# Performance work log

Measured on AMD Instinct MI355X. Metric: run time of the kernel, lower is better.

## Reference

```python
import jax, jax.numpy as jnp
import numpy as np

N = 512          # n_nodes
F = 64           # hidden scalar/vector channels (hidden_irreps 64x0e+64x1o)
S = 5            # num_species
T = 32           # time embedding dim
M = 64           # MLP_irreps 64x0e
L = 2            # num_interactions
AVG = 511.0      # avg_num_neighbors (fully connected)
E = N * (N - 1)


def _sph(v):
    """Real spherical harmonics l=0,1,2 (component norm) of normalized vectors. v: [E,3]."""
    r = jnp.linalg.norm(v, axis=-1, keepdims=True)  # [E,1]
    u = v / r
    x, y, z = u[..., 0], u[..., 1], u[..., 2]
    s3, s5, s15 = 3.0 ** 0.5, 5.0 ** 0.5, 15.0 ** 0.5
    Y0 = jnp.ones_like(x)[..., None]
    Y1 = s3 * u
    Y2 = jnp.stack([s15 * x * y, s15 * y * z, 0.5 * s5 * (3 * z * z - 1.0),
                    s15 * x * z, 0.5 * s15 * (x * x - y * y)], axis=-1)
    return jnp.concatenate([Y0, Y1, Y2], axis=-1), r  # [E,9], [E,1]


def setup_inputs() -> dict:
    key = jax.random.key(0)
    ks = jax.random.split(key, 16)
    snd, rcv = np.nonzero(~np.eye(N, dtype=bool))  # fully-connected, no self loops
    return dict(
        positions=jax.random.normal(ks[0], (N, 3), jnp.float32),
        node_features=jax.random.randint(ks[1], (N,), 1, S + 1, jnp.int32),
        time_embedding=jax.random.normal(ks[2], (T,), jnp.float32),
        senders=jnp.asarray(snd, jnp.int32),
        receivers=jnp.asarray(rcv, jnp.int32),
        W_embed=jax.random.normal(ks[3], (S + T, F)) * 0.1,
        b_embed=jnp.zeros((F,)),
        W_lin=jax.random.normal(ks[4], (L, 3, F, F)) / jnp.sqrt(float(F)),
        W_e1=jax.random.normal(ks[5], (L, 1, 32)),
        b_e1=jnp.zeros((L, 32)),
        W_e2=jax.random.normal(ks[6], (L, 32, F * 6)) * 0.05,
        Wp0=jax.random.normal(ks[7], (L, S, F, 6)) * 0.1,
        Wp1=jax.random.normal(ks[8], (L, S, F, 3)) * 0.1,
        Wr1=jax.random.normal(ks[9], (L, F, M)) / jnp.sqrt(float(F)),
        br1=jnp.zeros((L, M)),
        Wr2s=jax.random.normal(ks[10], (L, M, 16)) * 0.1,
        Wr2g=jax.random.normal(ks[11], (L, M, F)) * 0.1,
    )


def reference(positions, node_features, time_embedding, senders, receivers,
              W_embed, b_embed, W_lin, W_e1, b_e1, W_e2, Wp0, Wp1, Wr1, br1, Wr2s, Wr2g):
    species = node_features - 1                                  # ints in [0,S)
    onehot = jax.nn.one_hot(species, S, dtype=positions.dtype)   # /normalization_factor=1
    te = jnp.tile(time_embedding, (N, 1))
    h = jnp.concatenate([onehot, te], axis=-1) @ W_embed + b_embed  # embedding Dense -> [N,F]
    node_feats = jnp.zeros((N, F, 9), positions.dtype).at[:, :, 0].set(h)
    pos0 = positions
    pos = positions
    for l in range(L):
        vec = pos[receivers] - pos[senders]                      # [E,3]
        Y, lengths = _sph(vec)                                   # SH of edge dirs, edge lengths
        # per-l channel-mixing linear on node feats
        x0 = jnp.einsum('nf,fg->ng', node_feats[:, :, 0], W_lin[l, 0])
        x1 = jnp.einsum('nfm,fg->ngm', node_feats[:, :, 1:4], W_lin[l, 1])
        x2 = jnp.einsum('nfm,fg->ngm', node_feats[:, :, 4:9], W_lin[l, 2])
        s0, s1, s2 = x0[senders], x1[senders], x2[senders]       # gather sender feats
        # edge-length MLP producing per-channel per-CG-path weights
        he = jax.nn.silu(lengths @ W_e1[l] + b_e1[l])            # [E,32]
        w = (he @ W_e2[l]).reshape(-1, F, 6)                     # 6 TP paths
        Y1 = Y[:, None, 1:4]
        Y2c = Y[:, None, 4:9]
        # CG tensor-product paths: 0x0->0, 0x1->1, 0x2->2, 1x1->0, 1x1->1, 2x2->0
        m0 = (w[..., 0] * s0 * Y[:, 0:1]
              + w[..., 3] * jnp.sum(s1 * Y1, -1)
              + w[..., 5] * jnp.sum(s2 * Y2c, -1))               # [E,F]
        m1 = w[..., 1, None] * s0[..., None] * Y1 + w[..., 4, None] * jnp.cross(s1, Y1)
        m2 = w[..., 2, None] * s0[..., None] * Y2c
        msg = jnp.concatenate([m0[..., None], m1, m2], axis=-1)  # [E,F,9]
        A = jax.ops.segment_sum(msg, receivers, num_segments=N) / AVG  # scatter-aggregate
        # EquivariantProductBasisBlock: species-weighted symmetric contractions (correlation 3)
        A0, A1, A2 = A[:, :, 0], A[:, :, 1:4], A[:, :, 4:9]
        n1 = jnp.sum(A1 * A1, -1)
        n2 = jnp.sum(A2 * A2, -1)
        t0 = jnp.stack([A0, A0 * A0, A0 ** 3, n1, n2, A0 * n1], axis=-1)
        w0 = Wp0[l][species]                                     # [N,F,6]
        w1 = Wp1[l][species]                                     # [N,F,3]
        out0 = jnp.sum(t0 * w0, -1)                              # [N,F] scalars
        gpoly = w1[..., 0] + w1[..., 1] * A0 + w1[..., 2] * A0 * A0
        out1 = gpoly[..., None] * A1                             # [N,F,3] vectors
        node_feats = (jnp.zeros((N, F, 9), positions.dtype)
                      .at[:, :, 0].set(out0).at[:, :, 1:4].set(out1))
        # NonLinearReadoutBlock: gated vector readout (scalar outputs are discarded upstream)
        hr = jax.nn.silu(out0 @ Wr1[l] + br1[l])
        gate = hr @ Wr2g[l]                                      # [N,F]
        vec_out = jnp.einsum('nf,nfc->nc', gate, out1)           # [N,3] many_body_vectors
        pos = pos + vec_out
    return (pos - pos0)[:, :3]                                    # final_scaling = 1.0
```

## Files before the change

kernel.cpp:

```cpp
#include <hip/hip_runtime.h>
#include <hip/hip_bf16.h>

using bf16 = __hip_bfloat16;
using bf16x8 = __attribute__((ext_vector_type(8))) short;
using f32x4  = __attribute__((ext_vector_type(4))) float;

#define NN 512
#define NS 511

enum : int {
  WS_FLAG = 0,
  WS_X0S  = 16,
  WS_POS  = 336,
  WS_POS2 = 1872,
  WS_DELTA= 3408,
  WS_XS1  = 4960,
};

__device__ __forceinline__ short f2b(float x) {
  unsigned u = __builtin_bit_cast(unsigned, x);
  unsigned r = (u + 0x7fffu + ((u >> 16) & 1u)) >> 16;
  return (short)r;
}

__device__ __forceinline__ float ld(const void* p, int i, int isf32) {
  if (isf32) return ((const float*)p)[i];
  return __bfloat162float(((const bf16*)p)[i]);
}

__global__ __launch_bounds__(256) void k_pre(
    const void* __restrict__ positions, const void* __restrict__ te,
    const void* __restrict__ W_embed, const void* __restrict__ b_embed,
    const void* __restrict__ W_lin, float* __restrict__ ws) {
  const int b = blockIdx.x, t = threadIdx.x;
  __shared__ int flag_s;
  __shared__ float tvp[4][64];
  __shared__ float hst[64];
  __shared__ float xp[4][64];
  if (t < 64) {
    int cnt = 0;
    #pragma unroll
    for (int kq = 0; kq < 4; ++kq) {
      float v = __bfloat162float(((const bf16*)W_embed)[t + kq * 64]);
      float av = fabsf(v);
      cnt += (v == v && av > 1e-8f && av < 1e4f) ? 1 : 0;
    }
    #pragma unroll
    for (int off = 32; off > 0; off >>= 1) cnt += __shfl_down(cnt, off);
    if (t == 0) flag_s = (cnt >= 240) ? 0 : 1;
  }
  __syncthreads();
  const int isf32 = flag_s;

  if (b == 5) {
    if (t == 0) ((int*)ws)[WS_FLAG] = isf32;
    for (int idx = t; idx < NN * 3; idx += 256)
      ws[WS_POS + idx] = ld(positions, idx, isf32);
    return;
  }
  {
    int q = t & 63, kc = t >> 6;
    float ptv = 0.f;
    #pragma unroll
    for (int k = kc * 8; k < kc * 8 + 8; ++k)
      ptv += ld(te, k, isf32) * ld(W_embed, (5 + k) * 64 + q, isf32);
    tvp[kc][q] = ptv;
  }
  __syncthreads();
  if (t < 64)
    hst[t] = tvp[0][t] + tvp[1][t] + tvp[2][t] + tvp[3][t] +
             ld(b_embed, t, isf32) + ld(W_embed, b * 64 + t, isf32);
  __syncthreads();
  {
    int f = t & 63, qc = t >> 6;
    float px = 0.f;
    #pragma unroll
    for (int q2 = qc * 16; q2 < qc * 16 + 16; ++q2)
      px += hst[q2] * ld(W_lin, q2 * 64 + f, isf32);
    xp[qc][f] = px;
  }
  __syncthreads();
  if (t < 64)
    ws[WS_X0S + b * 64 + t] = xp[0][t] + xp[1][t] + xp[2][t] + xp[3][t];
}

template <int L>
__global__ __launch_bounds__(256) void k_edgenode(
    const int* __restrict__ nodef, const void* __restrict__ W_lin,
    const void* __restrict__ W_e1, const void* __restrict__ b_e1,
    const void* __restrict__ W_e2, const void* __restrict__ Wp0,
    const void* __restrict__ Wp1, const void* __restrict__ Wr1,
    const void* __restrict__ br1, const void* __restrict__ Wr2g,
    float* __restrict__ ws, void* __restrict__ out) {
  constexpr int HAS1 = L;
  constexpr int K = HAS1 ? 5 : 3;
  constexpr int N = K * 64;
  const int j = blockIdx.x;
  const int t = threadIdx.x;
  const int lane = t & 63;
  const int wave = t >> 6;
  const int quad = lane >> 4;
  const int lo = lane & 15;

  __shared__ short Bhi[N * 40];
  __shared__ float red[4][64][9];
  __shared__ float Af[64][9];
  __shared__ float s0l[64];
  __shared__ float o1l[3][64];
  __shared__ float hl[64];
  __shared__ float X0l[320];

  const int isf32 = ((const int*)ws)[WS_FLAG];

  {
    for (int idx = t; idx < N * 32; idx += 256) {
      int n = idx >> 5, h = idx & 31;
      int kp = n >> 6, f = n & 63;
      int src = (L * 32 + h) * 384 + f * 6 + kp;
      short bits;
      if (isf32) bits = f2b(((const float*)W_e2)[src]);
      else       bits = ((const short*)W_e2)[src];
      Bhi[n * 40 + h] = bits;
    }
    if (!HAS1) {
      for (int idx = t; idx < 320; idx += 256) X0l[idx] = ws[WS_X0S + idx];
    }
  }
  const float* pos = ws + (L ? WS_POS2 : WS_POS);
  const f32x4* xs = (const f32x4*)(ws + WS_XS1);
  float we1v[8], be1v[8];
  #pragma unroll
  for (int i = 0; i < 8; ++i) {
    we1v[i] = ld(W_e1, L * 32 + quad * 8 + i, isf32);
    be1v[i] = ld(b_e1, L * 32 + quad * 8 + i, isf32);
  }
  const float pjx = pos[j * 3 + 0], pjy = pos[j * 3 + 1], pjz = pos[j * 3 + 2];

  const float s3 = 1.7320508075688772f;
  const float s5h = 1.118033988749895f;
  const float s15 = 3.872983346207417f;
  const float s15h = 1.9364916731037085f;

  float acc[9][4] = {};
  __syncthreads();

  #pragma unroll 1
  for (int stile = wave; stile < 32; stile += 4) {
    bf16x8 af;
    {
      int ida = stile * 16 + lo;
      int ia = ida + (ida >= j);
      if (ia > 511) ia = 511;
      float pix = pos[ia * 3 + 0], piy = pos[ia * 3 + 1], piz = pos[ia * 3 + 2];
      float vx = pjx - pix, vy = pjy - piy, vz = pjz - piz;
      float r = sqrtf(vx * vx + vy * vy + vz * vz);
      #pragma unroll
      for (int i = 0; i < 8; ++i) {
        float x = r * we1v[i] + be1v[i];
        float he = x / (1.f + __expf(-x));
        af[i] = f2b(he);
      }
    }
    float Y1r[4][3], Y2r[4][5];
    int ir[4], sp4[4];
    bool vld[4];
    #pragma unroll
    for (int r4 = 0; r4 < 4; ++r4) {
      int idx = stile * 16 + quad * 4 + r4;
      vld[r4] = idx < NS;
      int i = idx + (idx >= j);
      if (i > 511) i = 511;
      ir[r4] = i;
      if (!HAS1) sp4[r4] = nodef[i] - 1;
      float pix = pos[i * 3 + 0], piy = pos[i * 3 + 1], piz = pos[i * 3 + 2];
      float vx = pjx - pix, vy = pjy - piy, vz = pjz - piz;
      float r2 = vx * vx + vy * vy + vz * vz;
      float rinv = r2 > 0.f ? rsqrtf(r2) : 0.f;
      float ux = vx * rinv, uy = vy * rinv, uz = vz * rinv;
      Y1r[r4][0] = s3 * ux; Y1r[r4][1] = s3 * uy; Y1r[r4][2] = s3 * uz;
      Y2r[r4][0] = s15 * ux * uy;
      Y2r[r4][1] = s15 * uy * uz;
      Y2r[r4][2] = s5h * (3.f * uz * uz - 1.f);
      Y2r[r4][3] = s15 * ux * uz;
      Y2r[r4][4] = s15h * (ux * ux - uy * uy);
    }
    #pragma unroll
    for (int ft = 0; ft < 4; ++ft) {
      int fcol = ft * 16 + lo;
      f32x4 xv[4];
      if (HAS1) {
        #pragma unroll
        for (int r4 = 0; r4 < 4; ++r4) xv[r4] = xs[ir[r4] * 64 + fcol];
      } else {
        #pragma unroll
        for (int r4 = 0; r4 < 4; ++r4) {
          f32x4 v = {X0l[sp4[r4] * 64 + fcol], 0.f, 0.f, 0.f};
          xv[r4] = v;
        }
      }
      f32x4 C[K];
      #pragma unroll
      for (int kp = 0; kp < K; ++kp) {
        const bf16x8 bh = *(const bf16x8*)&Bhi[(kp * 64 + fcol) * 40 + quad * 8];
        f32x4 c = {0.f, 0.f, 0.f, 0.f};
        C[kp] = __builtin_amdgcn_mfma_f32_16x16x32_bf16(af, bh, c, 0, 0, 0);
      }
      #pragma unroll
      for (int r4 = 0; r4 < 4; ++r4) {
        if (vld[r4]) {
          float s0 = xv[r4].x;
          float w0 = C[0][r4], w1 = C[1][r4], w2 = C[2][r4];
          if (HAS1) {
            float s1x = xv[r4].y, s1y = xv[r4].z, s1z = xv[r4].w;
            float w3 = C[3][r4], w4 = C[4][r4];
            float d1 = s1x * Y1r[r4][0] + s1y * Y1r[r4][1] + s1z * Y1r[r4][2];
            float cx = s1y * Y1r[r4][2] - s1z * Y1r[r4][1];
            float cy = s1z * Y1r[r4][0] - s1x * Y1r[r4][2];
            float cz = s1x * Y1r[r4][1] - s1y * Y1r[r4][0];
            acc[0][ft] += w0 * s0 + w3 * d1;
            float t1 = w1 * s0;
            acc[1][ft] += t1 * Y1r[r4][0] + w4 * cx;
            acc[2][ft] += t1 * Y1r[r4][1] + w4 * cy;
            acc[3][ft] += t1 * Y1r[r4][2] + w4 * cz;
          } else {
            acc[0][ft] += w0 * s0;
            float t1 = w1 * s0;
            acc[1][ft] += t1 * Y1r[r4][0];
            acc[2][ft] += t1 * Y1r[r4][1];
            acc[3][ft] += t1 * Y1r[r4][2];
          }
          float t2 = w2 * s0;
          acc[4][ft] += t2 * Y2r[r4][0];
          acc[5][ft] += t2 * Y2r[r4][1];
          acc[6][ft] += t2 * Y2r[r4][2];
          acc[7][ft] += t2 * Y2r[r4][3];
          acc[8][ft] += t2 * Y2r[r4][4];
        }
      }
    }
  }

  #pragma unroll
  for (int c = 0; c < 9; ++c)
    #pragma unroll
    for (int ft = 0; ft < 4; ++ft) {
      float v = acc[c][ft];
      v += __shfl_xor(v, 16);
      v += __shfl_xor(v, 32);
      acc[c][ft] = v;
    }
  if (quad == 0) {
    #pragma unroll
    for (int c = 0; c < 9; ++c)
      #pragma unroll
      for (int ft = 0; ft < 4; ++ft)
        red[wave][ft * 16 + lo][c] = acc[c][ft];
  }
  __syncthreads();
  for (int o = t; o < 576; o += 256) {
    int f = o / 9, c = o % 9;
    Af[f][c] = (red[0][f][c] + red[1][f][c] + red[2][f][c] + red[3][f][c]) *
               (1.f / 511.f);
  }
  __syncthreads();

  float out0 = 0.f, o1x = 0.f, o1y = 0.f, o1z = 0.f;
  if (t < 64) {
    int f = t;
    float a[9];
    #pragma unroll
    for (int c = 0; c < 9; ++c) a[c] = Af[f][c];
    int sp = nodef[j] - 1;
    int b0i = ((L * 5 + sp) * 64 + f) * 6;
    int b1i = ((L * 5 + sp) * 64 + f) * 3;
    float A0 = a[0];
    float n1 = a[1] * a[1] + a[2] * a[2] + a[3] * a[3];
    float n2 = a[4] * a[4] + a[5] * a[5] + a[6] * a[6] + a[7] * a[7] + a[8] * a[8];
    float A02 = A0 * A0;
    out0 = ld(Wp0, b0i + 0, isf32) * A0 + ld(Wp0, b0i + 1, isf32) * A02 +
           ld(Wp0, b0i + 2, isf32) * A02 * A0 + ld(Wp0, b0i + 3, isf32) * n1 +
           ld(Wp0, b0i + 4, isf32) * n2 + ld(Wp0, b0i + 5, isf32) * A0 * n1;
    float gp = ld(Wp1, b1i + 0, isf32) + ld(Wp1, b1i + 1, isf32) * A0 +
               ld(Wp1, b1i + 2, isf32) * A02;
    o1x = gp * a[1]; o1y = gp * a[2]; o1z = gp * a[3];
    s0l[f] = out0;
    if (L == 0) { o1l[0][f] = o1x; o1l[1][f] = o1y; o1l[2][f] = o1z; }
  }
  __syncthreads();
  if (t < 64) {
    int f = t;
    if (L == 0) {
      float b0 = 0.f, bx = 0.f, by = 0.f, bz = 0.f;
      #pragma unroll 8
      for (int q = 0; q < 64; ++q) {
        float w0 = ld(W_lin, 3 * 4096 + q * 64 + f, isf32);
        float w1 = ld(W_lin, 4 * 4096 + q * 64 + f, isf32);
        b0 += s0l[q] * w0;
        bx += o1l[0][q] * w1; by += o1l[1][q] * w1; bz += o1l[2][q] * w1;
      }
      f32x4 o = {b0, bx, by, bz};
      *(f32x4*)&ws[WS_XS1 + (j * 64 + f) * 4] = o;
    }
    float hacc = ld(br1, L * 64 + f, isf32);
    #pragma unroll 8
    for (int q = 0; q < 64; ++q)
      hacc += s0l[q] * ld(Wr1, (L * 64 + q) * 64 + f, isf32);
    hl[f] = hacc / (1.f + __expf(-hacc));
  }
  __syncthreads();
  if (t < 64) {
    int f = t;
    float gacc = 0.f;
    #pragma unroll 8
    for (int m = 0; m < 64; ++m)
      gacc += hl[m] * ld(Wr2g, (L * 64 + m) * 64 + f, isf32);
    float px = gacc * o1x, py = gacc * o1y, pz = gacc * o1z;
    #pragma unroll
    for (int off = 32; off > 0; off >>= 1) {
      px += __shfl_down(px, off);
      py += __shfl_down(py, off);
      pz += __shfl_down(pz, off);
    }
    if (f == 0) {
      if (L == 0) {
        ws[WS_DELTA + j * 3 + 0] = px;
        ws[WS_DELTA + j * 3 + 1] = py;
        ws[WS_DELTA + j * 3 + 2] = pz;
        ws[WS_POS2 + j * 3 + 0] = pos[j * 3 + 0] + px;
        ws[WS_POS2 + j * 3 + 1] = pos[j * 3 + 1] + py;
        ws[WS_POS2 + j * 3 + 2] = pos[j * 3 + 2] + pz;
      } else {
        float ox = ws[WS_DELTA + j * 3 + 0] + px;
        float oy = ws[WS_DELTA + j * 3 + 1] + py;
        float oz = ws[WS_DELTA + j * 3 + 2] + pz;
        if (isf32) {
          float* o = (float*)out;
          o[j * 3 + 0] = ox; o[j * 3 + 1] = oy; o[j * 3 + 2] = oz;
        } else {
          bf16* o = (bf16*)out;
          o[j * 3 + 0] = __float2bfloat16(ox);
          o[j * 3 + 1] = __float2bfloat16(oy);
          o[j * 3 + 2] = __float2bfloat16(oz);
        }
      }
    }
  }
}

extern "C" void kernel_launch(void* const* d_in, const int* in_sizes, int n_in,
                              void* d_out, int out_size, void* d_ws, size_t ws_size,
                              hipStream_t stream) {
  const void* positions = d_in[0];
  const int*  nodef     = (const int*)d_in[1];
  const void* te        = d_in[2];
  const void* W_embed   = d_in[5];
  const void* b_embed   = d_in[6];
  const void* W_lin     = d_in[7];
  const void* W_e1      = d_in[8];
  const void* b_e1      = d_in[9];
  const void* W_e2      = d_in[10];
  const void* Wp0       = d_in[11];
  const void* Wp1       = d_in[12];
  const void* Wr1       = d_in[13];
  const void* br1       = d_in[14];
  const void* Wr2g      = d_in[16];
  float* ws = (float*)d_ws;
  (void)in_sizes; (void)n_in; (void)out_size; (void)ws_size;

  k_pre<<<dim3(6), dim3(256), 0, stream>>>(positions, te, W_embed, b_embed,
                                           W_lin, ws);
  k_edgenode<0><<<dim3(512), dim3(256), 0, stream>>>(
      nodef, W_lin, W_e1, b_e1, W_e2, Wp0, Wp1, Wr1, br1, Wr2g, ws, d_out);
  k_edgenode<1><<<dim3(512), dim3(256), 0, stream>>>(
      nodef, W_lin, W_e1, b_e1, W_e2, Wp0, Wp1, Wr1, br1, Wr2g, ws, d_out);
}
```

Before: 187.6 us.

## Fold preprocessing kernel into edge-node kernels and parallelize node-tail matvecs

Removes the small k_pre launch: every block of the first edge kernel now redundantly computes the dtype flag, converts positions and species into shared memory, and computes the per-species initial embeddings. Positions are staged in LDS in both layers, so the edge loop reads them from shared memory instead of global. The per-node tail matvecs (W_lin, Wr1, Wr2g), previously done by a single wave, are split across all four waves with a shared-memory reduction. This trades one kernel launch and its serialization for redundant per-block setup work and extra LDS and barriers.

Result: slower. 205.1 us (+9.4%).

```diff
diff --git a/kernel.cpp b/kernel.cpp
--- a/kernel.cpp
+++ b/kernel.cpp
@@ -9,12 +9,9 @@
 #define NS 511
 
 enum : int {
-  WS_FLAG = 0,
-  WS_X0S  = 16,
-  WS_POS  = 336,
-  WS_POS2 = 1872,
-  WS_DELTA= 3408,
-  WS_XS1  = 4960,
+  WS_POS2 = 0,
+  WS_DELTA = 1536,
+  WS_XS1 = 3072,
 };
 
 __device__ __forceinline__ short f2b(float x) {
@@ -28,65 +25,11 @@
   return __bfloat162float(((const bf16*)p)[i]);
 }
 
-__global__ __launch_bounds__(256) void k_pre(
-    const void* __restrict__ positions, const void* __restrict__ te,
-    const void* __restrict__ W_embed, const void* __restrict__ b_embed,
-    const void* __restrict__ W_lin, float* __restrict__ ws) {
-  const int b = blockIdx.x, t = threadIdx.x;
-  __shared__ int flag_s;
-  __shared__ float tvp[4][64];
-  __shared__ float hst[64];
-  __shared__ float xp[4][64];
-  if (t < 64) {
-    int cnt = 0;
-    #pragma unroll
-    for (int kq = 0; kq < 4; ++kq) {
-      float v = __bfloat162float(((const bf16*)W_embed)[t + kq * 64]);
-      float av = fabsf(v);
-      cnt += (v == v && av > 1e-8f && av < 1e4f) ? 1 : 0;
-    }
-    #pragma unroll
-    for (int off = 32; off > 0; off >>= 1) cnt += __shfl_down(cnt, off);
-    if (t == 0) flag_s = (cnt >= 240) ? 0 : 1;
-  }
-  __syncthreads();
-  const int isf32 = flag_s;
-
-  if (b == 5) {
-    if (t == 0) ((int*)ws)[WS_FLAG] = isf32;
-    for (int idx = t; idx < NN * 3; idx += 256)
-      ws[WS_POS + idx] = ld(positions, idx, isf32);
-    return;
-  }
-  {
-    int q = t & 63, kc = t >> 6;
-    float ptv = 0.f;
-    #pragma unroll
-    for (int k = kc * 8; k < kc * 8 + 8; ++k)
-      ptv += ld(te, k, isf32) * ld(W_embed, (5 + k) * 64 + q, isf32);
-    tvp[kc][q] = ptv;
-  }
-  __syncthreads();
-  if (t < 64)
-    hst[t] = tvp[0][t] + tvp[1][t] + tvp[2][t] + tvp[3][t] +
-             ld(b_embed, t, isf32) + ld(W_embed, b * 64 + t, isf32);
-  __syncthreads();
-  {
-    int f = t & 63, qc = t >> 6;
-    float px = 0.f;
-    #pragma unroll
-    for (int q2 = qc * 16; q2 < qc * 16 + 16; ++q2)
-      px += hst[q2] * ld(W_lin, q2 * 64 + f, isf32);
-    xp[qc][f] = px;
-  }
-  __syncthreads();
-  if (t < 64)
-    ws[WS_X0S + b * 64 + t] = xp[0][t] + xp[1][t] + xp[2][t] + xp[3][t];
-}
-
 template <int L>
 __global__ __launch_bounds__(256) void k_edgenode(
-    const int* __restrict__ nodef, const void* __restrict__ W_lin,
+    const void* __restrict__ positions, const int* __restrict__ nodef,
+    const void* __restrict__ te, const void* __restrict__ W_embed,
+    const void* __restrict__ b_embed, const void* __restrict__ W_lin,
     const void* __restrict__ W_e1, const void* __restrict__ b_e1,
     const void* __restrict__ W_e2, const void* __restrict__ Wp0,
     const void* __restrict__ Wp1, const void* __restrict__ Wr1,
@@ -108,25 +51,73 @@
   __shared__ float s0l[64];
   __shared__ float o1l[3][64];
   __shared__ float hl[64];
+  __shared__ float posl[NN * 3];
   __shared__ float X0l[320];
-
-  const int isf32 = ((const int*)ws)[WS_FLAG];
-
-  {
-    for (int idx = t; idx < N * 32; idx += 256) {
-      int n = idx >> 5, h = idx & 31;
-      int kp = n >> 6, f = n & 63;
-      int src = (L * 32 + h) * 384 + f * 6 + kp;
-      short bits;
-      if (isf32) bits = f2b(((const float*)W_e2)[src]);
-      else       bits = ((const short*)W_e2)[src];
-      Bhi[n * 40 + h] = bits;
-    }
-    if (!HAS1) {
-      for (int idx = t; idx < 320; idx += 256) X0l[idx] = ws[WS_X0S + idx];
-    }
-  }
-  const float* pos = ws + (L ? WS_POS2 : WS_POS);
+  __shared__ int spl[NN];
+  __shared__ int flag_s;
+
+  if (t < 64) {
+    int cnt = 0;
+    #pragma unroll
+    for (int kq = 0; kq < 4; ++kq) {
+      float v = __bfloat162float(((const bf16*)W_embed)[t + kq * 64]);
+      float av = fabsf(v);
+      cnt += (v == v && av > 1e-8f && av < 1e4f) ? 1 : 0;
+    }
+    #pragma unroll
+    for (int off = 32; off > 0; off >>= 1) cnt += __shfl_down(cnt, off);
+    if (t == 0) flag_s = (cnt >= 240) ? 0 : 1;
+  }
+  __syncthreads();
+  const int isf32 = flag_s;
+
+  float* scr = &red[0][0][0];
+
+  if (!HAS1) {
+    for (int idx = t; idx < NN * 3; idx += 256)
+      posl[idx] = ld(positions, idx, isf32);
+    for (int idx = t; idx < NN; idx += 256) spl[idx] = nodef[idx] - 1;
+    {
+      int q = t & 63, kc = t >> 6;
+      float ptv = 0.f;
+      #pragma unroll
+      for (int k = kc * 8; k < kc * 8 + 8; ++k)
+        ptv += ld(te, k, isf32) * ld(W_embed, (5 + k) * 64 + q, isf32);
+      scr[kc * 64 + q] = ptv;
+    }
+  } else {
+    for (int idx = t; idx < NN * 3; idx += 256) posl[idx] = ws[WS_POS2 + idx];
+  }
+  for (int idx = t; idx < N * 32; idx += 256) {
+    int n = idx >> 5, h = idx & 31;
+    int kp = n >> 6, f = n & 63;
+    int src = (L * 32 + h) * 384 + f * 6 + kp;
+    short bits;
+    if (isf32) bits = f2b(((const float*)W_e2)[src]);
+    else       bits = ((const short*)W_e2)[src];
+    Bhi[n * 40 + h] = bits;
+  }
+  if (!HAS1) {
+    __syncthreads();
+    if (t < 64)
+      scr[512 + t] = scr[t] + scr[64 + t] + scr[128 + t] + scr[192 + t] +
+                     ld(b_embed, t, isf32);
+    __syncthreads();
+    for (int idx = t; idx < 320; idx += 256) {
+      int sp = idx >> 6, q = idx & 63;
+      scr[1024 + idx] = ld(W_embed, sp * 64 + q, isf32) + scr[512 + q];
+    }
+    __syncthreads();
+    for (int idx = t; idx < 320; idx += 256) {
+      int sp = idx >> 6, f = idx & 63;
+      float x = 0.f;
+      #pragma unroll 8
+      for (int q = 0; q < 64; ++q)
+        x += scr[1024 + sp * 64 + q] * ld(W_lin, q * 64 + f, isf32);
+      X0l[idx] = x;
+    }
+  }
+
   const f32x4* xs = (const f32x4*)(ws + WS_XS1);
   float we1v[8], be1v[8];
   #pragma unroll
@@ -134,15 +125,15 @@
     we1v[i] = ld(W_e1, L * 32 + quad * 8 + i, isf32);
     be1v[i] = ld(b_e1, L * 32 + quad * 8 + i, isf32);
   }
-  const float pjx = pos[j * 3 + 0], pjy = pos[j * 3 + 1], pjz = pos[j * 3 + 2];
 
   const float s3 = 1.7320508075688772f;
   const float s5h = 1.118033988749895f;
   const float s15 = 3.872983346207417f;
   const float s15h = 1.9364916731037085f;
 
+  __syncthreads();
+  const float pjx = posl[j * 3 + 0], pjy = posl[j * 3 + 1], pjz = posl[j * 3 + 2];
   float acc[9][4] = {};
-  __syncthreads();
 
   #pragma unroll 1
   for (int stile = wave; stile < 32; stile += 4) {
@@ -151,7 +142,7 @@
       int ida = stile * 16 + lo;
       int ia = ida + (ida >= j);
       if (ia > 511) ia = 511;
-      float pix = pos[ia * 3 + 0], piy = pos[ia * 3 + 1], piz = pos[ia * 3 + 2];
+      float pix = posl[ia * 3 + 0], piy = posl[ia * 3 + 1], piz = posl[ia * 3 + 2];
       float vx = pjx - pix, vy = pjy - piy, vz = pjz - piz;
       float r = sqrtf(vx * vx + vy * vy + vz * vz);
       #pragma unroll
@@ -171,8 +162,8 @@
       int i = idx + (idx >= j);
       if (i > 511) i = 511;
       ir[r4] = i;
-      if (!HAS1) sp4[r4] = nodef[i] - 1;
-      float pix = pos[i * 3 + 0], piy = pos[i * 3 + 1], piz = pos[i * 3 + 2];
+      if (!HAS1) sp4[r4] = spl[i];
+      float pix = posl[i * 3 + 0], piy = posl[i * 3 + 1], piz = posl[i * 3 + 2];
       float vx = pjx - pix, vy = pjy - piy, vz = pjz - piz;
       float r2 = vx * vx + vy * vy + vz * vz;
       float rinv = r2 > 0.f ? rsqrtf(r2) : 0.f;
@@ -287,33 +278,53 @@
     if (L == 0) { o1l[0][f] = o1x; o1l[1][f] = o1y; o1l[2][f] = o1z; }
   }
   __syncthreads();
+  {
+    int f = t & 63, qc = t >> 6;
+    float b0 = 0.f, bx = 0.f, by = 0.f, bz = 0.f, hacc = 0.f;
+    #pragma unroll 8
+    for (int q = qc * 16; q < qc * 16 + 16; ++q) {
+      float s0q = s0l[q];
+      if (L == 0) {
+        float w0 = ld(W_lin, 3 * 4096 + q * 64 + f, isf32);
+        float w1 = ld(W_lin, 4 * 4096 + q * 64 + f, isf32);
+        b0 += s0q * w0;
+        bx += o1l[0][q] * w1; by += o1l[1][q] * w1; bz += o1l[2][q] * w1;
+      }
+      hacc += s0q * ld(Wr1, (L * 64 + q) * 64 + f, isf32);
+    }
+    red[qc][f][0] = hacc;
+    if (L == 0) {
+      red[qc][f][1] = b0; red[qc][f][2] = bx;
+      red[qc][f][3] = by; red[qc][f][4] = bz;
+    }
+  }
+  __syncthreads();
   if (t < 64) {
     int f = t;
     if (L == 0) {
-      float b0 = 0.f, bx = 0.f, by = 0.f, bz = 0.f;
-      #pragma unroll 8
-      for (int q = 0; q < 64; ++q) {
-        float w0 = ld(W_lin, 3 * 4096 + q * 64 + f, isf32);
-        float w1 = ld(W_lin, 4 * 4096 + q * 64 + f, isf32);
-        b0 += s0l[q] * w0;
-        bx += o1l[0][q] * w1; by += o1l[1][q] * w1; bz += o1l[2][q] * w1;
-      }
-      f32x4 o = {b0, bx, by, bz};
+      f32x4 o = {red[0][f][1] + red[1][f][1] + red[2][f][1] + red[3][f][1],
+                 red[0][f][2] + red[1][f][2] + red[2][f][2] + red[3][f][2],
+                 red[0][f][3] + red[1][f][3] + red[2][f][3] + red[3][f][3],
+                 red[0][f][4] + red[1][f][4] + red[2][f][4] + red[3][f][4]};
       *(f32x4*)&ws[WS_XS1 + (j * 64 + f) * 4] = o;
     }
-    float hacc = ld(br1, L * 64 + f, isf32);
+    float hacc = red[0][f][0] + red[1][f][0] + red[2][f][0] + red[3][f][0] +
+                 ld(br1, L * 64 + f, isf32);
+    hl[f] = hacc / (1.f + __expf(-hacc));
+  }
+  __syncthreads();
+  {
+    int f = t & 63, mc = t >> 6;
+    float gacc = 0.f;
     #pragma unroll 8
-    for (int q = 0; q < 64; ++q)
-      hacc += s0l[q] * ld(Wr1, (L * 64 + q) * 64 + f, isf32);
-    hl[f] = hacc / (1.f + __expf(-hacc));
+    for (int m = mc * 16; m < mc * 16 + 16; ++m)
+      gacc += hl[m] * ld(Wr2g, (L * 64 + m) * 64 + f, isf32);
+    red[mc][f][0] = gacc;
   }
   __syncthreads();
   if (t < 64) {
     int f = t;
-    float gacc = 0.f;
-    #pragma unroll 8
-    for (int m = 0; m < 64; ++m)
-      gacc += hl[m] * ld(Wr2g, (L * 64 + m) * 64 + f, isf32);
+    float gacc = red[0][f][0] + red[1][f][0] + red[2][f][0] + red[3][f][0];
     float px = gacc * o1x, py = gacc * o1y, pz = gacc * o1z;
     #pragma unroll
     for (int off = 32; off > 0; off >>= 1) {
@@ -326,9 +337,9 @@
         ws[WS_DELTA + j * 3 + 0] = px;
         ws[WS_DELTA + j * 3 + 1] = py;
         ws[WS_DELTA + j * 3 + 2] = pz;
-        ws[WS_POS2 + j * 3 + 0] = pos[j * 3 + 0] + px;
-        ws[WS_POS2 + j * 3 + 1] = pos[j * 3 + 1] + py;
-        ws[WS_POS2 + j * 3 + 2] = pos[j * 3 + 2] + pz;
+        ws[WS_POS2 + j * 3 + 0] = posl[j * 3 + 0] + px;
+        ws[WS_POS2 + j * 3 + 1] = posl[j * 3 + 1] + py;
+        ws[WS_POS2 + j * 3 + 2] = posl[j * 3 + 2] + pz;
       } else {
         float ox = ws[WS_DELTA + j * 3 + 0] + px;
         float oy = ws[WS_DELTA + j * 3 + 1] + py;
@@ -367,10 +378,10 @@
   float* ws = (float*)d_ws;
   (void)in_sizes; (void)n_in; (void)out_size; (void)ws_size;
 
-  k_pre<<<dim3(6), dim3(256), 0, stream>>>(positions, te, W_embed, b_embed,
-                                           W_lin, ws);
   k_edgenode<0><<<dim3(512), dim3(256), 0, stream>>>(
-      nodef, W_lin, W_e1, b_e1, W_e2, Wp0, Wp1, Wr1, br1, Wr2g, ws, d_out);
+      positions, nodef, te, W_embed, b_embed, W_lin, W_e1, b_e1, W_e2, Wp0,
+      Wp1, Wr1, br1, Wr2g, ws, d_out);
   k_edgenode<1><<<dim3(512), dim3(256), 0, stream>>>(
-      nodef, W_lin, W_e1, b_e1, W_e2, Wp0, Wp1, Wr1, br1, Wr2g, ws, d_out);
+      positions, nodef, te, W_embed, b_embed, W_lin, W_e1, b_e1, W_e2, Wp0,
+      Wp1, Wr1, br1, Wr2g, ws, d_out);
 }
```

## Fuse pre and both interaction layers into one cooperative kernel with grid sync

Applied to the files above, without the earlier changes.

Moves the preprocessing and the two per-layer edge/node kernels into device functions and calls them from a single cooperative kernel, with grid-wide syncs between stages. Shared memory is unified into one struct that all stages reuse. The goal is to remove two kernel launch gaps and the tail drain between dependent launches. It falls back to the three-launch path if occupancy cannot hold all 512 blocks at once, and it adds grid-barrier cost plus possible register pressure from the fused kernel.

Result: no change. 189.6 us (+1.1%).

```diff
diff --git a/kernel.cpp b/kernel.cpp
--- a/kernel.cpp
+++ b/kernel.cpp
@@ -1,5 +1,8 @@
 #include <hip/hip_runtime.h>
 #include <hip/hip_bf16.h>
+#include <hip/hip_cooperative_groups.h>
+
+namespace cg = cooperative_groups;
 
 using bf16 = __hip_bfloat16;
 using bf16x8 = __attribute__((ext_vector_type(8))) short;
@@ -28,15 +31,24 @@
   return __bfloat162float(((const bf16*)p)[i]);
 }
 
-__global__ __launch_bounds__(256) void k_pre(
-    const void* __restrict__ positions, const void* __restrict__ te,
-    const void* __restrict__ W_embed, const void* __restrict__ b_embed,
-    const void* __restrict__ W_lin, float* __restrict__ ws) {
-  const int b = blockIdx.x, t = threadIdx.x;
-  __shared__ int flag_s;
-  __shared__ float tvp[4][64];
-  __shared__ float hst[64];
-  __shared__ float xp[4][64];
+struct SB {
+  short Bhi[320 * 40];
+  float red[4][64][9];
+  float Af[64][9];
+  float s0l[64];
+  float o1l[3][64];
+  float hl[64];
+  float X0l[320];
+  int   flag;
+};
+
+__device__ __forceinline__ void pre_body(
+    int b, int t, float* scr, int* flagp,
+    const void* positions, const void* te, const void* W_embed,
+    const void* b_embed, const void* W_lin, float* ws) {
+  float* tvp = scr;
+  float* hst = scr + 256;
+  float* xp  = scr + 320;
   if (t < 64) {
     int cnt = 0;
     #pragma unroll
@@ -47,45 +59,46 @@
     }
     #pragma unroll
     for (int off = 32; off > 0; off >>= 1) cnt += __shfl_down(cnt, off);
-    if (t == 0) flag_s = (cnt >= 240) ? 0 : 1;
-  }
-  __syncthreads();
-  const int isf32 = flag_s;
+    if (t == 0) *flagp = (cnt >= 240) ? 0 : 1;
+  }
+  __syncthreads();
+  const int isf32 = *flagp;
 
   if (b == 5) {
     if (t == 0) ((int*)ws)[WS_FLAG] = isf32;
     for (int idx = t; idx < NN * 3; idx += 256)
       ws[WS_POS + idx] = ld(positions, idx, isf32);
-    return;
-  }
-  {
-    int q = t & 63, kc = t >> 6;
-    float ptv = 0.f;
-    #pragma unroll
-    for (int k = kc * 8; k < kc * 8 + 8; ++k)
-      ptv += ld(te, k, isf32) * ld(W_embed, (5 + k) * 64 + q, isf32);
-    tvp[kc][q] = ptv;
-  }
-  __syncthreads();
-  if (t < 64)
-    hst[t] = tvp[0][t] + tvp[1][t] + tvp[2][t] + tvp[3][t] +
-             ld(b_embed, t, isf32) + ld(W_embed, b * 64 + t, isf32);
-  __syncthreads();
-  {
-    int f = t & 63, qc = t >> 6;
-    float px = 0.f;
-    #pragma unroll
-    for (int q2 = qc * 16; q2 < qc * 16 + 16; ++q2)
-      px += hst[q2] * ld(W_lin, q2 * 64 + f, isf32);
-    xp[qc][f] = px;
-  }
-  __syncthreads();
-  if (t < 64)
-    ws[WS_X0S + b * 64 + t] = xp[0][t] + xp[1][t] + xp[2][t] + xp[3][t];
+  } else {
+    {
+      int q = t & 63, kc = t >> 6;
+      float ptv = 0.f;
+      #pragma unroll
+      for (int k = kc * 8; k < kc * 8 + 8; ++k)
+        ptv += ld(te, k, isf32) * ld(W_embed, (5 + k) * 64 + q, isf32);
+      tvp[kc * 64 + q] = ptv;
+    }
+    __syncthreads();
+    if (t < 64)
+      hst[t] = tvp[t] + tvp[64 + t] + tvp[128 + t] + tvp[192 + t] +
+               ld(b_embed, t, isf32) + ld(W_embed, b * 64 + t, isf32);
+    __syncthreads();
+    {
+      int f = t & 63, qc = t >> 6;
+      float px = 0.f;
+      #pragma unroll
+      for (int q2 = qc * 16; q2 < qc * 16 + 16; ++q2)
+        px += hst[q2] * ld(W_lin, q2 * 64 + f, isf32);
+      xp[qc * 64 + f] = px;
+    }
+    __syncthreads();
+    if (t < 64)
+      ws[WS_X0S + b * 64 + t] = xp[t] + xp[64 + t] + xp[128 + t] + xp[192 + t];
+  }
 }
 
 template <int L>
-__global__ __launch_bounds__(256) void k_edgenode(
+__device__ __forceinline__ void edge_body(
+    int j, int t, SB& s,
     const int* __restrict__ nodef, const void* __restrict__ W_lin,
     const void* __restrict__ W_e1, const void* __restrict__ b_e1,
     const void* __restrict__ W_e2, const void* __restrict__ Wp0,
@@ -95,20 +108,10 @@
   constexpr int HAS1 = L;
   constexpr int K = HAS1 ? 5 : 3;
   constexpr int N = K * 64;
-  const int j = blockIdx.x;
-  const int t = threadIdx.x;
   const int lane = t & 63;
   const int wave = t >> 6;
   const int quad = lane >> 4;
   const int lo = lane & 15;
-
-  __shared__ short Bhi[N * 40];
-  __shared__ float red[4][64][9];
-  __shared__ float Af[64][9];
-  __shared__ float s0l[64];
-  __shared__ float o1l[3][64];
-  __shared__ float hl[64];
-  __shared__ float X0l[320];
 
   const int isf32 = ((const int*)ws)[WS_FLAG];
 
@@ -120,10 +123,10 @@
       short bits;
       if (isf32) bits = f2b(((const float*)W_e2)[src]);
       else       bits = ((const short*)W_e2)[src];
-      Bhi[n * 40 + h] = bits;
+      s.Bhi[n * 40 + h] = bits;
     }
     if (!HAS1) {
-      for (int idx = t; idx < 320; idx += 256) X0l[idx] = ws[WS_X0S + idx];
+      for (int idx = t; idx < 320; idx += 256) s.X0l[idx] = ws[WS_X0S + idx];
     }
   }
   const float* pos = ws + (L ? WS_POS2 : WS_POS);
@@ -194,14 +197,14 @@
       } else {
         #pragma unroll
         for (int r4 = 0; r4 < 4; ++r4) {
-          f32x4 v = {X0l[sp4[r4] * 64 + fcol], 0.f, 0.f, 0.f};
+          f32x4 v = {s.X0l[sp4[r4] * 64 + fcol], 0.f, 0.f, 0.f};
           xv[r4] = v;
         }
       }
       f32x4 C[K];
       #pragma unroll
       for (int kp = 0; kp < K; ++kp) {
-        const bf16x8 bh = *(const bf16x8*)&Bhi[(kp * 64 + fcol) * 40 + quad * 8];
+        const bf16x8 bh = *(const bf16x8*)&s.Bhi[(kp * 64 + fcol) * 40 + quad * 8];
         f32x4 c = {0.f, 0.f, 0.f, 0.f};
         C[kp] = __builtin_amdgcn_mfma_f32_16x16x32_bf16(af, bh, c, 0, 0, 0);
       }
@@ -254,13 +257,13 @@
     for (int c = 0; c < 9; ++c)
       #pragma unroll
       for (int ft = 0; ft < 4; ++ft)
-        red[wave][ft * 16 + lo][c] = acc[c][ft];
+        s.red[wave][ft * 16 + lo][c] = acc[c][ft];
   }
   __syncthreads();
   for (int o = t; o < 576; o += 256) {
     int f = o / 9, c = o % 9;
-    Af[f][c] = (red[0][f][c] + red[1][f][c] + red[2][f][c] + red[3][f][c]) *
-               (1.f / 511.f);
+    s.Af[f][c] = (s.red[0][f][c] + s.red[1][f][c] + s.red[2][f][c] +
+                  s.red[3][f][c]) * (1.f / 511.f);
   }
   __syncthreads();
 
@@ -269,7 +272,7 @@
     int f = t;
     float a[9];
     #pragma unroll
-    for (int c = 0; c < 9; ++c) a[c] = Af[f][c];
+    for (int c = 0; c < 9; ++c) a[c] = s.Af[f][c];
     int sp = nodef[j] - 1;
     int b0i = ((L * 5 + sp) * 64 + f) * 6;
     int b1i = ((L * 5 + sp) * 64 + f) * 3;
@@ -283,8 +286,8 @@
     float gp = ld(Wp1, b1i + 0, isf32) + ld(Wp1, b1i + 1, isf32) * A0 +
                ld(Wp1, b1i + 2, isf32) * A02;
     o1x = gp * a[1]; o1y = gp * a[2]; o1z = gp * a[3];
-    s0l[f] = out0;
-    if (L == 0) { o1l[0][f] = o1x; o1l[1][f] = o1y; o1l[2][f] = o1z; }
+    s.s0l[f] = out0;
+    if (L == 0) { s.o1l[0][f] = o1x; s.o1l[1][f] = o1y; s.o1l[2][f] = o1z; }
   }
   __syncthreads();
   if (t < 64) {
@@ -295,8 +298,8 @@
       for (int q = 0; q < 64; ++q) {
         float w0 = ld(W_lin, 3 * 4096 + q * 64 + f, isf32);
         float w1 = ld(W_lin, 4 * 4096 + q * 64 + f, isf32);
-        b0 += s0l[q] * w0;
-        bx += o1l[0][q] * w1; by += o1l[1][q] * w1; bz += o1l[2][q] * w1;
+        b0 += s.s0l[q] * w0;
+        bx += s.o1l[0][q] * w1; by += s.o1l[1][q] * w1; bz += s.o1l[2][q] * w1;
       }
       f32x4 o = {b0, bx, by, bz};
       *(f32x4*)&ws[WS_XS1 + (j * 64 + f) * 4] = o;
@@ -304,8 +307,8 @@
     float hacc = ld(br1, L * 64 + f, isf32);
     #pragma unroll 8
     for (int q = 0; q < 64; ++q)
-      hacc += s0l[q] * ld(Wr1, (L * 64 + q) * 64 + f, isf32);
-    hl[f] = hacc / (1.f + __expf(-hacc));
+      hacc += s.s0l[q] * ld(Wr1, (L * 64 + q) * 64 + f, isf32);
+    s.hl[f] = hacc / (1.f + __expf(-hacc));
   }
   __syncthreads();
   if (t < 64) {
@@ -313,7 +316,7 @@
     float gacc = 0.f;
     #pragma unroll 8
     for (int m = 0; m < 64; ++m)
-      gacc += hl[m] * ld(Wr2g, (L * 64 + m) * 64 + f, isf32);
+      gacc += s.hl[m] * ld(Wr2g, (L * 64 + m) * 64 + f, isf32);
     float px = gacc * o1x, py = gacc * o1y, pz = gacc * o1z;
     #pragma unroll
     for (int off = 32; off > 0; off >>= 1) {
@@ -347,6 +350,48 @@
   }
 }
 
+__global__ __launch_bounds__(256) void k_pre(
+    const void* __restrict__ positions, const void* __restrict__ te,
+    const void* __restrict__ W_embed, const void* __restrict__ b_embed,
+    const void* __restrict__ W_lin, float* __restrict__ ws) {
+  __shared__ float scr[576];
+  __shared__ int flag;
+  pre_body(blockIdx.x, threadIdx.x, scr, &flag, positions, te, W_embed,
+           b_embed, W_lin, ws);
+}
+
+template <int L>
+__global__ __launch_bounds__(256) void k_edgenode(
+    const int* __restrict__ nodef, const void* __restrict__ W_lin,
+    const void* __restrict__ W_e1, const void* __restrict__ b_e1,
+    const void* __restrict__ W_e2, const void* __restrict__ Wp0,
+    const void* __restrict__ Wp1, const void* __restrict__ Wr1,
+    const void* __restrict__ br1, const void* __restrict__ Wr2g,
+    float* __restrict__ ws, void* __restrict__ out) {
+  __shared__ SB s;
+  edge_body<L>(blockIdx.x, threadIdx.x, s, nodef, W_lin, W_e1, b_e1, W_e2,
+               Wp0, Wp1, Wr1, br1, Wr2g, ws, out);
+}
+
+__global__ __launch_bounds__(256) void k_fused(
+    const void* positions, const int* nodef, const void* te,
+    const void* W_embed, const void* b_embed, const void* W_lin,
+    const void* W_e1, const void* b_e1, const void* W_e2,
+    const void* Wp0, const void* Wp1, const void* Wr1, const void* br1,
+    const void* Wr2g, float* ws, void* out) {
+  __shared__ SB s;
+  cg::grid_group g = cg::this_grid();
+  if (blockIdx.x < 6)
+    pre_body(blockIdx.x, threadIdx.x, &s.red[0][0][0], &s.flag,
+             positions, te, W_embed, b_embed, W_lin, ws);
+  g.sync();
+  edge_body<0>(blockIdx.x, threadIdx.x, s, nodef, W_lin, W_e1, b_e1, W_e2,
+               Wp0, Wp1, Wr1, br1, Wr2g, ws, out);
+  g.sync();
+  edge_body<1>(blockIdx.x, threadIdx.x, s, nodef, W_lin, W_e1, b_e1, W_e2,
+               Wp0, Wp1, Wr1, br1, Wr2g, ws, out);
+}
+
 extern "C" void kernel_launch(void* const* d_in, const int* in_sizes, int n_in,
                               void* d_out, int out_size, void* d_ws, size_t ws_size,
                               hipStream_t stream) {
@@ -367,10 +412,35 @@
   float* ws = (float*)d_ws;
   (void)in_sizes; (void)n_in; (void)out_size; (void)ws_size;
 
-  k_pre<<<dim3(6), dim3(256), 0, stream>>>(positions, te, W_embed, b_embed,
-                                           W_lin, ws);
-  k_edgenode<0><<<dim3(512), dim3(256), 0, stream>>>(
-      nodef, W_lin, W_e1, b_e1, W_e2, Wp0, Wp1, Wr1, br1, Wr2g, ws, d_out);
-  k_edgenode<1><<<dim3(512), dim3(256), 0, stream>>>(
-      nodef, W_lin, W_e1, b_e1, W_e2, Wp0, Wp1, Wr1, br1, Wr2g, ws, d_out);
-}
+  static int coop = -1;
+  if (coop < 0) {
+    int dev = 0;
+    (void)hipGetDevice(&dev);
+    int ncu = 0;
+    (void)hipDeviceGetAttribute(&ncu, hipDeviceAttributeMultiprocessorCount, dev);
+    int maxb = 0;
+    hipError_t qe = hipOccupancyMaxActiveBlocksPerMultiprocessor(
+        &maxb, reinterpret_cast<const void*>(k_fused), 256, 0);
+    coop = (qe == hipSuccess && ncu > 0 && (long)maxb * ncu >= 512) ? 1 : 0;
+  }
+
+  bool launched = false;
+  if (coop == 1) {
+    void* args[] = {&positions, &nodef, &te, &W_embed, &b_embed, &W_lin,
+                    &W_e1, &b_e1, &W_e2, &Wp0, &Wp1, &Wr1, &br1, &Wr2g,
+                    &ws, &d_out};
+    hipError_t e = hipLaunchCooperativeKernel(
+        reinterpret_cast<const void*>(k_fused), dim3(512), dim3(256), args, 0,
+        stream);
+    if (e == hipSuccess) launched = true;
+    else coop = 0;
+  }
+  if (!launched) {
+    k_pre<<<dim3(6), dim3(256), 0, stream>>>(positions, te, W_embed, b_embed,
+                                             W_lin, ws);
+    k_edgenode<0><<<dim3(512), dim3(256), 0, stream>>>(
+        nodef, W_lin, W_e1, b_e1, W_e2, Wp0, Wp1, Wr1, br1, Wr2g, ws, d_out);
+    k_edgenode<1><<<dim3(512), dim3(256), 0, stream>>>(
+        nodef, W_lin, W_e1, b_e1, W_e2, Wp0, Wp1, Wr1, br1, Wr2g, ws, d_out);
+  }
+}
```
